# Performance work log

Measured on AMD Instinct MI355X. Metric: run time of the kernel, lower is better.

Reference implementation:

```python
import jax, jax.numpy as jnp
import numpy as np

N, D, C, T = 4096, 1024, 1000, 32  # tokens, n_embd, n_class, n_logit_samples


def setup_inputs() -> dict:
    key = jax.random.key(0)
    k1, k2 = jax.random.split(key)
    x = jax.random.normal(k1, (N, D), dtype=jnp.float32)
    # 0.02 init scale keeps exp(logvar) numerically sane (standard GPT-style init)
    W = jax.random.normal(k2, (2 * C, D), dtype=jnp.float32) * 0.02
    return {"x": x, "W": W}


def reference(x, W):
    # linear head (bias-free): [N, D] @ [D, 2C] -> [N, 2C]
    h = jnp.einsum('nd,cd->nc', x, W)
    mu, logvar = h[:, :C], h[:, C:]
    sigma = jnp.exp(0.5 * logvar)  # sqrt(exp(logvar))

    # MC sampling of logits, vectorized over the T sample loop.
    # torch subtracts the row max before softmax; that is exactly what a
    # numerically-stable softmax does, so the math is identical.
    eps = jax.random.normal(jax.random.key(42), (T, N, C), dtype=mu.dtype)
    logits = mu[None] + sigma[None] * eps           # [T, N, C]
    probs = jax.nn.softmax(logits, axis=-1)         # [T, N, C]
    prob = jnp.mean(probs, axis=0)                  # [N, C]
    mu_out = jnp.exp(prob)                          # faithful to torch.exp(prob)
    return (mu_out, sigma)
```

## Files before the change

### kernel.cpp

```cpp
#include <hip/hip_runtime.h>


typedef __attribute__((ext_vector_type(8))) _Float16 f16x8;
typedef __attribute__((ext_vector_type(4))) float f32x4;
typedef __attribute__((ext_vector_type(2))) float f32x2;

#define NC_TOT  4096000
#define H_HALF  65536000u

__device__ __forceinline__ unsigned short f2h(float f) {
  _Float16 h = (_Float16)f;
  return __builtin_bit_cast(unsigned short, h);
}

__global__ __launch_bounds__(256) void convert_kernel(
    const float* __restrict__ x, const float* __restrict__ W,
    unsigned short* __restrict__ xh, unsigned short* __restrict__ wh) {
  int qid = blockIdx.x * 256 + threadIdx.x;
  if (qid < 1048576) {
    float4 v = ((const float4*)x)[qid];
    ushort4 o = make_ushort4(f2h(v.x), f2h(v.y), f2h(v.z), f2h(v.w));
    ((ushort4*)xh)[qid] = o;
  } else {
    int q = qid - 1048576;
    int row = q >> 8;
    ushort4 o;
    if (row < 2000) {
      float4 v = ((const float4*)W)[q];
      o = make_ushort4(f2h(v.x), f2h(v.y), f2h(v.z), f2h(v.w));
    } else {
      o = make_ushort4(0, 0, 0, 0);
    }
    ((ushort4*)wh)[q] = o;
  }
}

#define BK  32
#define LDK 40

__global__ __launch_bounds__(256) void gemm_kernel(
    const unsigned short* __restrict__ Ah,
    const unsigned short* __restrict__ Bh,
    float* __restrict__ mu,
    float* __restrict__ sigma_out) {
  const int K = 1024;
  __shared__ unsigned short As[128 * LDK];
  __shared__ unsigned short Bs[128 * LDK];

  int tid  = threadIdx.x;
  int bx   = blockIdx.x;
  int by   = blockIdx.y;
  int w    = tid >> 6;
  int lane = tid & 63;
  int wr   = (w >> 1) * 64;
  int wc   = (w & 1) * 64;
  int lrow = lane & 15;
  int kq   = lane >> 4;

  f32x4 acc[4][4];
  for (int i = 0; i < 4; i++)
    for (int j = 0; j < 4; j++) acc[i][j] = (f32x4){0.f, 0.f, 0.f, 0.f};

  int srow = tid >> 2;
  int sq   = tid & 3;
  int aBase = (by * 128) * K;
  int bBase = (bx * 128) * K;

  for (int kk = 0; kk < K; kk += BK) {
    uint4 av0 = *(const uint4*)(Ah + aBase + srow * K        + kk + sq * 8);
    uint4 av1 = *(const uint4*)(Ah + aBase + (srow + 64) * K + kk + sq * 8);
    uint4 bv0 = *(const uint4*)(Bh + bBase + srow * K        + kk + sq * 8);
    uint4 bv1 = *(const uint4*)(Bh + bBase + (srow + 64) * K + kk + sq * 8);
    __syncthreads();
    *(uint4*)(As + srow * LDK        + sq * 8) = av0;
    *(uint4*)(As + (srow + 64) * LDK + sq * 8) = av1;
    *(uint4*)(Bs + srow * LDK        + sq * 8) = bv0;
    *(uint4*)(Bs + (srow + 64) * LDK + sq * 8) = bv1;
    __syncthreads();

    f16x8 a[4], b[4];
    for (int i = 0; i < 4; i++)
      a[i] = *(const f16x8*)(As + (wr + i * 16 + lrow) * LDK + kq * 8);
    for (int j = 0; j < 4; j++)
      b[j] = *(const f16x8*)(Bs + (wc + j * 16 + lrow) * LDK + kq * 8);
    for (int i = 0; i < 4; i++)
      for (int j = 0; j < 4; j++)
        acc[i][j] = __builtin_amdgcn_mfma_f32_16x16x32_f16(a[i], b[j], acc[i][j], 0, 0, 0);
  }

  int orow0 = by * 128 + wr + (lane >> 4) * 4;
  int ocol0 = bx * 128 + wc + (lane & 15);
  for (int i = 0; i < 4; i++) {
    for (int j = 0; j < 4; j++) {
      int c = ocol0 + j * 16;
      for (int v = 0; v < 4; v++) {
        int r = orow0 + i * 16 + v;
        float val = acc[i][j][v];
        if (c < 1000)       mu[r * 1000 + c] = val;
        else if (c < 2000)  sigma_out[r * 1000 + (c - 1000)] = __expf(0.5f * val);
      }
    }
  }
}

__device__ __forceinline__ void threefry(unsigned x0, unsigned x1,
                                         unsigned& o0, unsigned& o1) {
  const unsigned ks1 = 42u;
  const unsigned ks2 = 0x1BD11BDAu ^ 42u;
#define TF_RND(r) { x0 += x1; x1 = (x1 << (r)) | (x1 >> (32 - (r))); x1 ^= x0; }
  x1 += ks1;
  TF_RND(13) TF_RND(15) TF_RND(26) TF_RND(6)
  x0 += ks1;  x1 += ks2 + 1u;
  TF_RND(17) TF_RND(29) TF_RND(16) TF_RND(24)
  x0 += ks2;  x1 += 2u;
  TF_RND(13) TF_RND(15) TF_RND(26) TF_RND(6)
  x1 += ks1 + 3u;
  TF_RND(17) TF_RND(29) TF_RND(16) TF_RND(24)
  x0 += ks1;  x1 += ks2 + 4u;
  TF_RND(13) TF_RND(15) TF_RND(26) TF_RND(6)
  x0 += ks2;  x1 += 5u;
#undef TF_RND
  o0 = x0; o1 = x1;
}

__device__ __forceinline__ float erfinv_big(float x, float w) {
  float v = __fsqrt_rn(w) - 3.0f;
  float p = -0.000200214257f;
  p = fmaf(p, v, 0.000100950558f);
  p = fmaf(p, v, 0.00134934322f);
  p = fmaf(p, v, -0.00367342844f);
  p = fmaf(p, v, 0.00573950773f);
  p = fmaf(p, v, -0.0076224613f);
  p = fmaf(p, v, 0.00943887047f);
  p = fmaf(p, v, 1.00167406f);
  p = fmaf(p, v, 2.83297682f);
  return 1.41421356f * (p * x);
}

__device__ __forceinline__ f32x2 splat2(float c) { return (f32x2){c, c}; }

__device__ __forceinline__ f32x2 normal2(f32x2 x) {
  f32x2 t = __builtin_elementwise_fma(-x, x, splat2(1.0f));
  f32x2 lg;
  lg.x = __builtin_amdgcn_logf(t.x);
  lg.y = __builtin_amdgcn_logf(t.y);
  f32x2 w = lg * splat2(-0.69314718f);
  f32x2 v = w - splat2(2.5f);
  f32x2 p = splat2(2.81022636e-08f);
  p = __builtin_elementwise_fma(p, v, splat2(3.43273939e-07f));
  p = __builtin_elementwise_fma(p, v, splat2(-3.5233877e-06f));
  p = __builtin_elementwise_fma(p, v, splat2(-4.39150654e-06f));
  p = __builtin_elementwise_fma(p, v, splat2(0.00021858087f));
  p = __builtin_elementwise_fma(p, v, splat2(-0.00125372503f));
  p = __builtin_elementwise_fma(p, v, splat2(-0.00417768164f));
  p = __builtin_elementwise_fma(p, v, splat2(0.246640727f));
  p = __builtin_elementwise_fma(p, v, splat2(1.50140941f));
  f32x2 r = (p * x) * splat2(1.41421356f);
  if (w.x >= 5.0f) r.x = erfinv_big(x.x, w.x);
  if (w.y >= 5.0f) r.y = erfinv_big(x.y, w.y);
  return r;
}

__device__ __forceinline__ f32x2 bits_to_u2(unsigned b0, unsigned b1) {
  f32x2 f;
  f.x = __builtin_bit_cast(float, (b0 >> 9) | 0x3f800000u);
  f.y = __builtin_bit_cast(float, (b1 >> 9) | 0x3f800000u);
  f = f - splat2(1.0f);
  f32x2 u = __builtin_elementwise_fma(f, splat2(2.0f), splat2(-0.99999994f));
  return __builtin_elementwise_max(u, splat2(-0.99999994f));
}

__global__ __launch_bounds__(256) void sample_kernel(
    const float* __restrict__ mu,
    const float* __restrict__ sigma,
    float* __restrict__ out0) {
  int n    = blockIdx.x;
  int tid  = threadIdx.x;
  int lane = tid & 63, w = tid >> 6;
  __shared__ float pbuf[4][1024];

  int cb = n * 1000;
  float muv[16], sgv[16], prob[16];
#pragma unroll
  for (int j = 0; j < 16; j++) {
    int c = j * 64 + lane;
    bool val = (c < 1000);
    muv[j] = val ? mu[cb + c]    : 0.f;
    sgv[j] = val ? sigma[cb + c] : 0.f;
    prob[j] = 0.f;
  }

  float eA[16], eB[16];
#pragma unroll 1
  for (int it = 0; it < 4; it++) {
    int t = w * 4 + it;
    unsigned ib = (unsigned)(t * 4096000 + cb) + (unsigned)lane;
    float sA = 0.f, sB = 0.f;
#pragma unroll
    for (int j = 0; j < 16; j++) {
      unsigned i0 = ib + (unsigned)(j * 64);
      unsigned o0, o1;
      threefry(i0, i0 + H_HALF, o0, o1);
      f32x2 eps = normal2(bits_to_u2(o0, o1));
      float a = __expf(fmaf(sgv[j], eps.x, muv[j]));
      float b = __expf(fmaf(sgv[j], eps.y, muv[j]));
      if (j == 15) {
        a = (lane < 40) ? a : 0.f;
        b = (lane < 40) ? b : 0.f;
      }
      eA[j] = a; eB[j] = b;
      sA += a; sB += b;
    }
#pragma unroll
    for (int m = 1; m < 64; m <<= 1) {
      sA += __shfl_xor(sA, m, 64);
      sB += __shfl_xor(sB, m, 64);
    }
    float rA = 1.0f / sA, rB = 1.0f / sB;
#pragma unroll
    for (int j = 0; j < 16; j++)
      prob[j] = fmaf(eA[j], rA, fmaf(eB[j], rB, prob[j]));
  }

#pragma unroll
  for (int j = 0; j < 16; j++)
    pbuf[w][j * 64 + lane] = prob[j];
  __syncthreads();
#pragma unroll
  for (int k = 0; k < 4; k++) {
    int c = tid + k * 256;
    if (c < 1000) {
      float s = pbuf[0][c] + pbuf[1][c] + pbuf[2][c] + pbuf[3][c];
      out0[cb + c] = __expf(s * 0.03125f);
    }
  }
}

extern "C" void kernel_launch(void* const* d_in, const int* in_sizes, int n_in,
                              void* d_out, int out_size, void* d_ws, size_t ws_size,
                              hipStream_t stream) {
  const float* x = (const float*)d_in[0];
  const float* W = (const float*)d_in[1];
  float* out = (float*)d_out;

  unsigned short* xh = (unsigned short*)d_ws;
  unsigned short* wh = (unsigned short*)((char*)d_ws + 8388608);
  float*          mu = (float*)((char*)d_ws + 12582912);
  float* sigma = out + NC_TOT;

  convert_kernel<<<6144, 256, 0, stream>>>(x, W, xh, wh);
  dim3 g2(16, 32);
  gemm_kernel<<<g2, 256, 0, stream>>>(xh, wh, mu, sigma);
  sample_kernel<<<4096, 256, 0, stream>>>(mu, sigma, out);
}
```

Baseline: 291.3 us.

## Use direct global-to-LDS loads in GEMM and pack sampling math into float2

The GEMM tile loads now go straight from global memory into LDS through global_load_lds, replacing the register staging. The LDS padding is dropped, so the tile rows are now unpadded at a 32-element stride, which may bring back bank conflicts on the MFMA operand reads. The sampling kernel packs the fma and the running sum into float2 vectors, removes the clamp on the uniform value, and adds a min-blocks launch bound of 4 to steer register allocation. Dropping the clamp could change edge-case numerics.

```diff
diff --git a/kernel.cpp b/kernel.cpp
--- a/kernel.cpp
+++ b/kernel.cpp
@@ -19,8 +19,7 @@
   int qid = blockIdx.x * 256 + threadIdx.x;
   if (qid < 1048576) {
     float4 v = ((const float4*)x)[qid];
-    ushort4 o = make_ushort4(f2h(v.x), f2h(v.y), f2h(v.z), f2h(v.w));
-    ((ushort4*)xh)[qid] = o;
+    ((ushort4*)xh)[qid] = make_ushort4(f2h(v.x), f2h(v.y), f2h(v.z), f2h(v.w));
   } else {
     int q = qid - 1048576;
     int row = q >> 8;
@@ -35,8 +34,14 @@
   }
 }
 
-#define BK  32
-#define LDK 40
+#define BK 32
+
+typedef __attribute__((address_space(3))) unsigned char lds_byte;
+typedef __attribute__((address_space(1))) unsigned char glb_byte;
+
+__device__ __forceinline__ void glds16(const unsigned short* g, unsigned short* l) {
+  __builtin_amdgcn_global_load_lds((const glb_byte*)g, (lds_byte*)l, 16, 0, 0);
+}
 
 __global__ __launch_bounds__(256) void gemm_kernel(
     const unsigned short* __restrict__ Ah,
@@ -44,8 +49,8 @@
     float* __restrict__ mu,
     float* __restrict__ sigma_out) {
   const int K = 1024;
-  __shared__ unsigned short As[128 * LDK];
-  __shared__ unsigned short Bs[128 * LDK];
+  __shared__ unsigned short As[128 * BK];
+  __shared__ unsigned short Bs[128 * BK];
 
   int tid  = threadIdx.x;
   int bx   = blockIdx.x;
@@ -61,28 +66,26 @@
   for (int i = 0; i < 4; i++)
     for (int j = 0; j < 4; j++) acc[i][j] = (f32x4){0.f, 0.f, 0.f, 0.f};
 
-  int srow = tid >> 2;
-  int sq   = tid & 3;
-  int aBase = (by * 128) * K;
-  int bBase = (bx * 128) * K;
+  int srow = w * 16 + (lane >> 2);
+  int scol = (lane & 3) * 8;
+  const unsigned short* Ap = Ah + (by * 128 + srow) * K + scol;
+  const unsigned short* Bp = Bh + (bx * 128 + srow) * K + scol;
+  unsigned short* lA = As + w * 512;
+  unsigned short* lB = Bs + w * 512;
 
   for (int kk = 0; kk < K; kk += BK) {
-    uint4 av0 = *(const uint4*)(Ah + aBase + srow * K        + kk + sq * 8);
-    uint4 av1 = *(const uint4*)(Ah + aBase + (srow + 64) * K + kk + sq * 8);
-    uint4 bv0 = *(const uint4*)(Bh + bBase + srow * K        + kk + sq * 8);
-    uint4 bv1 = *(const uint4*)(Bh + bBase + (srow + 64) * K + kk + sq * 8);
     __syncthreads();
-    *(uint4*)(As + srow * LDK        + sq * 8) = av0;
-    *(uint4*)(As + (srow + 64) * LDK + sq * 8) = av1;
-    *(uint4*)(Bs + srow * LDK        + sq * 8) = bv0;
-    *(uint4*)(Bs + (srow + 64) * LDK + sq * 8) = bv1;
+    glds16(Ap + kk,            lA);
+    glds16(Ap + kk + 64 * K,   lA + 2048);
+    glds16(Bp + kk,            lB);
+    glds16(Bp + kk + 64 * K,   lB + 2048);
     __syncthreads();
 
     f16x8 a[4], b[4];
     for (int i = 0; i < 4; i++)
-      a[i] = *(const f16x8*)(As + (wr + i * 16 + lrow) * LDK + kq * 8);
+      a[i] = *(const f16x8*)(As + (wr + i * 16 + lrow) * BK + kq * 8);
     for (int j = 0; j < 4; j++)
-      b[j] = *(const f16x8*)(Bs + (wc + j * 16 + lrow) * LDK + kq * 8);
+      b[j] = *(const f16x8*)(Bs + (wc + j * 16 + lrow) * BK + kq * 8);
     for (int i = 0; i < 4; i++)
       for (int j = 0; j < 4; j++)
         acc[i][j] = __builtin_amdgcn_mfma_f32_16x16x32_f16(a[i], b[j], acc[i][j], 0, 0, 0);
@@ -166,11 +169,10 @@
   f.x = __builtin_bit_cast(float, (b0 >> 9) | 0x3f800000u);
   f.y = __builtin_bit_cast(float, (b1 >> 9) | 0x3f800000u);
   f = f - splat2(1.0f);
-  f32x2 u = __builtin_elementwise_fma(f, splat2(2.0f), splat2(-0.99999994f));
-  return __builtin_elementwise_max(u, splat2(-0.99999994f));
-}
-
-__global__ __launch_bounds__(256) void sample_kernel(
+  return __builtin_elementwise_fma(f, splat2(2.0f), splat2(-0.99999994f));
+}
+
+__global__ __launch_bounds__(256, 4) void sample_kernel(
     const float* __restrict__ mu,
     const float* __restrict__ sigma,
     float* __restrict__ out0) {
@@ -190,36 +192,38 @@
     prob[j] = 0.f;
   }
 
-  float eA[16], eB[16];
+  f32x2 e[16];
 #pragma unroll 1
   for (int it = 0; it < 4; it++) {
     int t = w * 4 + it;
     unsigned ib = (unsigned)(t * 4096000 + cb) + (unsigned)lane;
-    float sA = 0.f, sB = 0.f;
+    f32x2 s = splat2(0.f);
 #pragma unroll
     for (int j = 0; j < 16; j++) {
       unsigned i0 = ib + (unsigned)(j * 64);
       unsigned o0, o1;
       threefry(i0, i0 + H_HALF, o0, o1);
       f32x2 eps = normal2(bits_to_u2(o0, o1));
-      float a = __expf(fmaf(sgv[j], eps.x, muv[j]));
-      float b = __expf(fmaf(sgv[j], eps.y, muv[j]));
+      f32x2 lg = __builtin_elementwise_fma(splat2(sgv[j]), eps, splat2(muv[j]));
+      f32x2 ev;
+      ev.x = __expf(lg.x);
+      ev.y = __expf(lg.y);
       if (j == 15) {
-        a = (lane < 40) ? a : 0.f;
-        b = (lane < 40) ? b : 0.f;
+        ev.x = (lane < 40) ? ev.x : 0.f;
+        ev.y = (lane < 40) ? ev.y : 0.f;
       }
-      eA[j] = a; eB[j] = b;
-      sA += a; sB += b;
+      e[j] = ev;
+      s = s + ev;
     }
 #pragma unroll
     for (int m = 1; m < 64; m <<= 1) {
-      sA += __shfl_xor(sA, m, 64);
-      sB += __shfl_xor(sB, m, 64);
-    }
-    float rA = 1.0f / sA, rB = 1.0f / sB;
+      s.x += __shfl_xor(s.x, m, 64);
+      s.y += __shfl_xor(s.y, m, 64);
+    }
+    float rA = 1.0f / s.x, rB = 1.0f / s.y;
 #pragma unroll
     for (int j = 0; j < 16; j++)
-      prob[j] = fmaf(eA[j], rA, fmaf(eB[j], rB, prob[j]));
+      prob[j] = fmaf(e[j].x, rA, fmaf(e[j].y, rB, prob[j]));
   }
 
 #pragma unroll
@@ -230,8 +234,8 @@
   for (int k = 0; k < 4; k++) {
     int c = tid + k * 256;
     if (c < 1000) {
-      float s = pbuf[0][c] + pbuf[1][c] + pbuf[2][c] + pbuf[3][c];
-      out0[cb + c] = __expf(s * 0.03125f);
+      float sm = pbuf[0][c] + pbuf[1][c] + pbuf[2][c] + pbuf[3][c];
+      out0[cb + c] = __expf(sm * 0.03125f);
     }
   }
 }
```

Result: no change. 289.8 us (-0.5%).
